# Kernel tuning notes

Hardware: AMD Instinct MI355X
Metric: run time of the kernel (lower is better)

Reference implementation:

```python
import jax, jax.numpy as jnp
import numpy as np

B, CIN, COUT, K, H, W = 16, 128, 256, 3, 56, 56
STRIDE = 1
PAD = K // 2


def setup_inputs() -> dict:
    key = jax.random.key(0)
    ks = jax.random.split(key, 12)
    x = jax.random.normal(ks[0], (B, CIN, H, W), dtype=jnp.float32)
    base_kernel = jax.random.normal(ks[1], (COUT, CIN, K, K), dtype=jnp.float32)
    bias = jnp.zeros((COUT,), dtype=jnp.float32)
    s = 1.0 / np.sqrt(CIN)
    fc_spatial_w = jax.random.uniform(ks[2], (K * K, CIN), minval=-s, maxval=s)
    fc_spatial_b = jax.random.uniform(ks[3], (K * K,), minval=-s, maxval=s)
    fc_in_w = jax.random.uniform(ks[4], (CIN, CIN), minval=-s, maxval=s)
    fc_in_b = jax.random.uniform(ks[5], (CIN,), minval=-s, maxval=s)
    fc_out_w = jax.random.uniform(ks[6], (COUT, CIN), minval=-s, maxval=s)
    fc_out_b = jax.random.uniform(ks[7], (COUT,), minval=-s, maxval=s)
    fc_kernel_w = jax.random.uniform(ks[8], (COUT * CIN * K * K, CIN), minval=-s, maxval=s)
    fc_kernel_b = jax.random.uniform(ks[9], (COUT * CIN * K * K,), minval=-s, maxval=s)
    return {
        "x": x, "base_kernel": base_kernel, "bias": bias,
        "fc_spatial_w": fc_spatial_w, "fc_spatial_b": fc_spatial_b,
        "fc_in_w": fc_in_w, "fc_in_b": fc_in_b,
        "fc_out_w": fc_out_w, "fc_out_b": fc_out_b,
        "fc_kernel_w": fc_kernel_w, "fc_kernel_b": fc_kernel_b,
    }


def _odconv(x, base_kernel, bias, fc_spatial_w, fc_spatial_b, fc_in_w, fc_in_b,
            fc_out_w, fc_out_b, fc_kernel_w, fc_kernel_b):
    b = x.shape[0]
    # global average pool -> context [B, Cin]
    context = jnp.mean(x, axis=(2, 3))
    sig = jax.nn.sigmoid
    attn_spatial = sig(context @ fc_spatial_w.T + fc_spatial_b).reshape(b, 1, 1, K, K)
    attn_in = sig(context @ fc_in_w.T + fc_in_b).reshape(b, 1, CIN, 1, 1)
    attn_out = sig(context @ fc_out_w.T + fc_out_b).reshape(b, COUT, 1, 1, 1)
    attn_kernel = sig(context @ fc_kernel_w.T + fc_kernel_b).reshape(b, COUT, CIN, K, K)
    # 5-way broadcast multiply -> per-sample dynamic kernel [B, Cout, Cin, K, K]
    dyn = base_kernel[None] * attn_out * attn_in * attn_spatial * attn_kernel

    def conv_one(xi, wi):
        # xi: [Cin, H, W], wi: [Cout, Cin, K, K]
        out = jax.lax.conv_general_dilated(
            xi[None], wi,
            window_strides=(STRIDE, STRIDE),
            padding=[(PAD, PAD), (PAD, PAD)],
            dimension_numbers=("NCHW", "OIHW", "NCHW"),
        )
        return out[0]

    out = jax.vmap(conv_one)(x, dyn)  # [B, Cout, H', W']
    return out + bias[None, :, None, None]


def reference(x, base_kernel, bias, fc_spatial_w, fc_spatial_b, fc_in_w, fc_in_b,
              fc_out_w, fc_out_b, fc_kernel_w, fc_kernel_b):
    return _odconv(x, base_kernel, bias, fc_spatial_w, fc_spatial_b, fc_in_w, fc_in_b,
                   fc_out_w, fc_out_b, fc_kernel_w, fc_kernel_b)
```

## Files before the change

### kernel.cpp

```cpp
#include <hip/hip_runtime.h>
#include <hip/hip_bf16.h>
#include <math.h>

#define BATCH 16
#define CIN   128
#define COUT  256
#define HH    56
#define WW    56
#define HW    3136
#define NTAP  9
#define NE    (COUT*CIN*NTAP)

typedef short short8 __attribute__((ext_vector_type(8)));
typedef float floatx4 __attribute__((ext_vector_type(4)));

#define WSB_CTX   0
#define WSB_ASP   8192
#define WSB_AIN   9472
#define WSB_AOUT  17664
#define WSB_XT    34048
#define WSB_DYN   (WSB_XT + BATCH*HW*CIN*2)

static __device__ inline unsigned short f2b(float f) {
    union { float f; unsigned u; } v; v.f = f;
    unsigned r = v.u + 0x7FFF + ((v.u >> 16) & 1);
    return (unsigned short)(r >> 16);
}
static __device__ inline short8 pack8(float4 a, float4 b) {
    short8 r;
    r[0] = (short)f2b(a.x); r[1] = (short)f2b(a.y); r[2] = (short)f2b(a.z); r[3] = (short)f2b(a.w);
    r[4] = (short)f2b(b.x); r[5] = (short)f2b(b.y); r[6] = (short)f2b(b.z); r[7] = (short)f2b(b.w);
    return r;
}

__global__ void k_context(const float* __restrict__ x, float* __restrict__ ctx) {
    int bc = blockIdx.x;
    const float4* p = (const float4*)(x + (size_t)bc * HW);
    float s = 0.f;
    for (int i = threadIdx.x; i < HW / 4; i += 256) { float4 v = p[i]; s += v.x + v.y + v.z + v.w; }
    for (int off = 32; off; off >>= 1) s += __shfl_down(s, off, 64);
    __shared__ float red[4];
    if ((threadIdx.x & 63) == 0) red[threadIdx.x >> 6] = s;
    __syncthreads();
    if (threadIdx.x == 0) ctx[bc] = (red[0] + red[1] + red[2] + red[3]) * (1.f / (float)HW);
}

__global__ void k_xt(const float* __restrict__ x, unsigned short* __restrict__ xt) {
    int b = blockIdx.y;
    int p = blockIdx.x * 64 + (threadIdx.x & 63);
    int icq = threadIdx.x >> 6;
    const float* xb = x + (size_t)b * CIN * HW + p;
    unsigned short tmp[32];
#pragma unroll
    for (int j = 0; j < 32; ++j) tmp[j] = f2b(xb[(size_t)(icq * 32 + j) * HW]);
    uint4* dst = (uint4*)(xt + ((size_t)b * HW + p) * CIN + icq * 32);
    const uint4* s = (const uint4*)tmp;
    dst[0] = s[0]; dst[1] = s[1]; dst[2] = s[2]; dst[3] = s[3];
}

__global__ void k_attn(const float* __restrict__ ctx,
                       const float* __restrict__ wsp, const float* __restrict__ bsp,
                       const float* __restrict__ win, const float* __restrict__ bin,
                       const float* __restrict__ wout, const float* __restrict__ bout,
                       float* __restrict__ asp, float* __restrict__ ain, float* __restrict__ aout) {
    int R = blockIdx.x * 4 + (threadIdx.x >> 6);
    int lane = threadIdx.x & 63;
    int b = R / 393, r = R % 393;
    const float* w; float bias; float* o;
    if (r < 9)        { w = wsp  + r * CIN;         bias = bsp[r];         o = asp  + b * 16  + r; }
    else if (r < 137) { w = win  + (r - 9) * CIN;   bias = bin[r - 9];     o = ain  + b * CIN + (r - 9); }
    else              { w = wout + (r - 137) * CIN; bias = bout[r - 137];  o = aout + b * COUT + (r - 137); }
    float2 wv = ((const float2*)w)[lane];
    float2 cv = ((const float2*)(ctx + b * CIN))[lane];
    float d = wv.x * cv.x + wv.y * cv.y;
    for (int off = 32; off; off >>= 1) d += __shfl_down(d, off, 64);
    if (lane == 0) *o = 1.f / (1.f + __expf(-(d + bias)));
}

__global__ void k_build(const float* __restrict__ ctx, const float* __restrict__ wk,
                        const float* __restrict__ bk, const float* __restrict__ base,
                        const float* __restrict__ asp, const float* __restrict__ ain,
                        const float* __restrict__ aout, unsigned short* __restrict__ dyn) {
    int wid = threadIdx.x >> 6, l = threadIdx.x & 63;
    int lq = l & 15, quad = l >> 4;
    short8 afr[4];
    const float* arow = ctx + lq * CIN;
#pragma unroll
    for (int kc = 0; kc < 4; ++kc) {
        float4 v0 = *(const float4*)(arow + kc * 32 + quad * 8);
        float4 v1 = *(const float4*)(arow + kc * 32 + quad * 8 + 4);
        afr[kc] = pack8(v0, v1);
    }
    int n0w = blockIdx.x * 512 + wid * 128;
    for (int nf = 0; nf < 8; ++nf) {
        int n0 = n0w + nf * 16;
        int ic  = (n0 & 127) + lq;
        int oc  = (n0 >> 7) & 255;
        int tap = n0 >> 15;
        int e = (oc * CIN + ic) * NTAP + tap;
        const float* wrow = wk + (size_t)e * CIN;
        floatx4 acc = {0.f, 0.f, 0.f, 0.f};
#pragma unroll
        for (int kc = 0; kc < 4; ++kc) {
            float4 v0 = *(const float4*)(wrow + kc * 32 + quad * 8);
            float4 v1 = *(const float4*)(wrow + kc * 32 + quad * 8 + 4);
            short8 bfr = pack8(v0, v1);
            acc = __builtin_amdgcn_mfma_f32_16x16x32_bf16(afr[kc], bfr, acc, 0, 0, 0);
        }
        float bke = bk[e], bse = base[e];
#pragma unroll
        for (int r = 0; r < 4; ++r) {
            int b = quad * 4 + r;
            float s = 1.f / (1.f + __expf(-(acc[r] + bke)));
            float v = bse * s * aout[b * COUT + oc] * ain[b * CIN + ic] * asp[b * 16 + tap];
            dyn[(size_t)b * NE + n0 + lq] = f2b(v);
        }
    }
}

__global__ __launch_bounds__(256, 2) void k_conv(
    const unsigned short* __restrict__ xt, const unsigned short* __restrict__ dyn,
    const float* __restrict__ bias, float* __restrict__ out) {
    __shared__ char s_x[348 * 80];
    __shared__ char s_a[2][128 * 80];
    int b = blockIdx.z, oc0 = blockIdx.y * 128, r0 = blockIdx.x * 4;
    int tid = threadIdx.x;
    int wid = tid >> 6, l = tid & 63, lq = l & 15, quad = l >> 4;
    int wm = wid & 1, wn = wid >> 1;
    const unsigned short* xtb  = xt  + (size_t)b * HW * CIN;
    const unsigned short* dynb = dyn + (size_t)b * NE;

    int pixaddr[7];
#pragma unroll
    for (int nf = 0; nf < 7; ++nf) {
        int n = wn * 112 + nf * 16 + lq;
        int ry = n / 56, cx = n % 56;
        pixaddr[nf] = (ry * 58 + cx) * 80 + quad * 16;
    }

    floatx4 acc[4][7];
#pragma unroll
    for (int i = 0; i < 4; ++i)
#pragma unroll
        for (int j = 0; j < 7; ++j) acc[i][j] = (floatx4){0.f, 0.f, 0.f, 0.f};

    for (int kc = 0; kc < 4; ++kc) {
        for (int u = tid; u < 1392; u += 256) {
            int icq = u & 3, pix = u >> 2;
            int ry = pix / 58, cx = pix % 58;
            int gy = r0 + ry - 1, gx = cx - 1;
            uint4 v = {0u, 0u, 0u, 0u};
            if (gy >= 0 && gy < HH && gx >= 0 && gx < WW)
                v = *(const uint4*)(xtb + (size_t)(gy * WW + gx) * CIN + kc * 32 + icq * 8);
            *(uint4*)(s_x + pix * 80 + icq * 16) = v;
        }
        for (int u = tid; u < 512; u += 256) {
            int icq = u & 3, oc = u >> 2;
            *(uint4*)(s_a[0] + oc * 80 + icq * 16) =
                *(const uint4*)(dynb + (size_t)(oc0 + oc) * CIN + kc * 32 + icq * 8);
        }
        __syncthreads();
#pragma unroll
        for (int tap = 0; tap < 9; ++tap) {
            if (tap < 8) {
                for (int u = tid; u < 512; u += 256) {
                    int icq = u & 3, oc = u >> 2;
                    *(uint4*)(s_a[(tap + 1) & 1] + oc * 80 + icq * 16) =
                        *(const uint4*)(dynb + (size_t)((tap + 1) * COUT + oc0 + oc) * CIN + kc * 32 + icq * 8);
                }
            }
            const char* sa = s_a[tap & 1];
            short8 af[4];
#pragma unroll
            for (int mf = 0; mf < 4; ++mf)
                af[mf] = *(const short8*)(sa + (wm * 64 + mf * 16 + lq) * 80 + quad * 16);
            int toff = ((tap / 3) * 58 + (tap % 3)) * 80;
#pragma unroll
            for (int nf = 0; nf < 7; ++nf) {
                short8 bf = *(const short8*)(s_x + pixaddr[nf] + toff);
#pragma unroll
                for (int mf = 0; mf < 4; ++mf)
                    acc[mf][nf] = __builtin_amdgcn_mfma_f32_16x16x32_bf16(af[mf], bf, acc[mf][nf], 0, 0, 0);
            }
            __syncthreads();
        }
    }

#pragma unroll
    for (int mf = 0; mf < 4; ++mf) {
#pragma unroll
        for (int r = 0; r < 4; ++r) {
            int oc = oc0 + wm * 64 + mf * 16 + quad * 4 + r;
            float bs = bias[oc];
            float* ob = out + (size_t)(b * COUT + oc) * HW + r0 * WW + wn * 112 + lq;
#pragma unroll
            for (int nf = 0; nf < 7; ++nf)
                ob[nf * 16] = acc[mf][nf][r] + bs;
        }
    }
}

extern "C" void kernel_launch(void* const* d_in, const int* in_sizes, int n_in,
                              void* d_out, int out_size, void* d_ws, size_t ws_size,
                              hipStream_t stream) {
    const float* x    = (const float*)d_in[0];
    const float* base = (const float*)d_in[1];
    const float* bias = (const float*)d_in[2];
    const float* wsp  = (const float*)d_in[3];
    const float* bsp  = (const float*)d_in[4];
    const float* win  = (const float*)d_in[5];
    const float* bin  = (const float*)d_in[6];
    const float* wout = (const float*)d_in[7];
    const float* bout = (const float*)d_in[8];
    const float* wk   = (const float*)d_in[9];
    const float* bk   = (const float*)d_in[10];
    float* out = (float*)d_out;
    char* ws = (char*)d_ws;

    float* ctx  = (float*)(ws + WSB_CTX);
    float* asp  = (float*)(ws + WSB_ASP);
    float* ain  = (float*)(ws + WSB_AIN);
    float* aout = (float*)(ws + WSB_AOUT);
    unsigned short* xt  = (unsigned short*)(ws + WSB_XT);
    unsigned short* dyn = (unsigned short*)(ws + WSB_DYN);

    k_context<<<BATCH * CIN, 256, 0, stream>>>(x, ctx);
    k_xt<<<dim3(HW / 64, BATCH), 256, 0, stream>>>(x, xt);
    k_attn<<<(BATCH * 393) / 4, 256, 0, stream>>>(ctx, wsp, bsp, win, bin, wout, bout, asp, ain, aout);
    k_build<<<NE / 512, 256, 0, stream>>>(ctx, wk, bk, base, asp, ain, aout, dyn);
    k_conv<<<dim3(HH / 4, COUT / 128, BATCH), 256, 0, stream>>>(xt, dyn, bias, out);
}
```

Measured before the change: 345.9 us.

## Retile conv to 8 rows x 64 channels, stage all taps per chunk

The conv kernel now covers 8 output rows by 64 output channels per block, with each wave owning two rows. Each input-channel chunk loads all 9 taps of weights into LDS at once, which removes the per-tap double-buffer loads and the per-tap barriers. The LDS row stride drops from 80 to 64 bytes, which risks more bank conflicts, and the weight-build kernel gets twice as many smaller blocks. Per-block LDS grows to about 73 KB, which may limit how many blocks fit on a CU.

Result: faster. 332.5 us (-3.9%).

```diff
diff --git a/kernel.cpp b/kernel.cpp
--- a/kernel.cpp
+++ b/kernel.cpp
@@ -91,8 +91,8 @@
         float4 v1 = *(const float4*)(arow + kc * 32 + quad * 8 + 4);
         afr[kc] = pack8(v0, v1);
     }
-    int n0w = blockIdx.x * 512 + wid * 128;
-    for (int nf = 0; nf < 8; ++nf) {
+    int n0w = blockIdx.x * 256 + wid * 64;
+    for (int nf = 0; nf < 4; ++nf) {
         int n0 = n0w + nf * 16;
         int ic  = (n0 & 127) + lq;
         int oc  = (n0 >> 7) & 255;
@@ -121,21 +121,20 @@
 __global__ __launch_bounds__(256, 2) void k_conv(
     const unsigned short* __restrict__ xt, const unsigned short* __restrict__ dyn,
     const float* __restrict__ bias, float* __restrict__ out) {
-    __shared__ char s_x[348 * 80];
-    __shared__ char s_a[2][128 * 80];
-    int b = blockIdx.z, oc0 = blockIdx.y * 128, r0 = blockIdx.x * 4;
+    __shared__ char s_x[580 * 64];
+    __shared__ char s_a[576 * 64];
+    int b = blockIdx.z, oc0 = blockIdx.y * 64, r0 = blockIdx.x * 8;
     int tid = threadIdx.x;
-    int wid = tid >> 6, l = tid & 63, lq = l & 15, quad = l >> 4;
-    int wm = wid & 1, wn = wid >> 1;
+    int wn = tid >> 6, l = tid & 63, lq = l & 15, quad = l >> 4;
     const unsigned short* xtb  = xt  + (size_t)b * HW * CIN;
     const unsigned short* dynb = dyn + (size_t)b * NE;
 
     int pixaddr[7];
 #pragma unroll
     for (int nf = 0; nf < 7; ++nf) {
-        int n = wn * 112 + nf * 16 + lq;
-        int ry = n / 56, cx = n % 56;
-        pixaddr[nf] = (ry * 58 + cx) * 80 + quad * 16;
+        int n = nf * 16 + lq;
+        int tr = wn * 2 + n / 56, col = n % 56;
+        pixaddr[nf] = (tr * 58 + col) * 64 + quad * 16;
     }
 
     floatx4 acc[4][7];
@@ -145,36 +144,29 @@
         for (int j = 0; j < 7; ++j) acc[i][j] = (floatx4){0.f, 0.f, 0.f, 0.f};
 
     for (int kc = 0; kc < 4; ++kc) {
-        for (int u = tid; u < 1392; u += 256) {
+        __syncthreads();
+        for (int u = tid; u < 2320; u += 256) {
             int icq = u & 3, pix = u >> 2;
             int ry = pix / 58, cx = pix % 58;
             int gy = r0 + ry - 1, gx = cx - 1;
             uint4 v = {0u, 0u, 0u, 0u};
             if (gy >= 0 && gy < HH && gx >= 0 && gx < WW)
                 v = *(const uint4*)(xtb + (size_t)(gy * WW + gx) * CIN + kc * 32 + icq * 8);
-            *(uint4*)(s_x + pix * 80 + icq * 16) = v;
-        }
-        for (int u = tid; u < 512; u += 256) {
-            int icq = u & 3, oc = u >> 2;
-            *(uint4*)(s_a[0] + oc * 80 + icq * 16) =
-                *(const uint4*)(dynb + (size_t)(oc0 + oc) * CIN + kc * 32 + icq * 8);
+            *(uint4*)(s_x + pix * 64 + icq * 16) = v;
+        }
+        for (int u = tid; u < 2304; u += 256) {
+            int icq = u & 3, oc = (u >> 2) & 63, tap = u >> 8;
+            *(uint4*)(s_a + u * 16) =
+                *(const uint4*)(dynb + (size_t)(tap * COUT + oc0 + oc) * CIN + kc * 32 + icq * 8);
         }
         __syncthreads();
 #pragma unroll
         for (int tap = 0; tap < 9; ++tap) {
-            if (tap < 8) {
-                for (int u = tid; u < 512; u += 256) {
-                    int icq = u & 3, oc = u >> 2;
-                    *(uint4*)(s_a[(tap + 1) & 1] + oc * 80 + icq * 16) =
-                        *(const uint4*)(dynb + (size_t)((tap + 1) * COUT + oc0 + oc) * CIN + kc * 32 + icq * 8);
-                }
-            }
-            const char* sa = s_a[tap & 1];
             short8 af[4];
 #pragma unroll
             for (int mf = 0; mf < 4; ++mf)
-                af[mf] = *(const short8*)(sa + (wm * 64 + mf * 16 + lq) * 80 + quad * 16);
-            int toff = ((tap / 3) * 58 + (tap % 3)) * 80;
+                af[mf] = *(const short8*)(s_a + (tap * 64 + mf * 16 + lq) * 64 + quad * 16);
+            int toff = ((tap / 3) * 58 + (tap % 3)) * 64;
 #pragma unroll
             for (int nf = 0; nf < 7; ++nf) {
                 short8 bf = *(const short8*)(s_x + pixaddr[nf] + toff);
@@ -182,7 +174,6 @@
                 for (int mf = 0; mf < 4; ++mf)
                     acc[mf][nf] = __builtin_amdgcn_mfma_f32_16x16x32_bf16(af[mf], bf, acc[mf][nf], 0, 0, 0);
             }
-            __syncthreads();
         }
     }
 
@@ -190,9 +181,9 @@
     for (int mf = 0; mf < 4; ++mf) {
 #pragma unroll
         for (int r = 0; r < 4; ++r) {
-            int oc = oc0 + wm * 64 + mf * 16 + quad * 4 + r;
+            int oc = oc0 + mf * 16 + quad * 4 + r;
             float bs = bias[oc];
-            float* ob = out + (size_t)(b * COUT + oc) * HW + r0 * WW + wn * 112 + lq;
+            float* ob = out + (size_t)(b * COUT + oc) * HW + (r0 + wn * 2) * 56 + lq;
 #pragma unroll
             for (int nf = 0; nf < 7; ++nf)
                 ob[nf * 16] = acc[mf][nf][r] + bs;
@@ -227,6 +218,6 @@
     k_context<<<BATCH * CIN, 256, 0, stream>>>(x, ctx);
     k_xt<<<dim3(HW / 64, BATCH), 256, 0, stream>>>(x, xt);
     k_attn<<<(BATCH * 393) / 4, 256, 0, stream>>>(ctx, wsp, bsp, win, bin, wout, bout, asp, ain, aout);
-    k_build<<<NE / 512, 256, 0, stream>>>(ctx, wk, bk, base, asp, ain, aout, dyn);
-    k_conv<<<dim3(HH / 4, COUT / 128, BATCH), 256, 0, stream>>>(xt, dyn, bias, out);
-}
+    k_build<<<NE / 256, 256, 0, stream>>>(ctx, wk, bk, base, asp, ain, aout, dyn);
+    k_conv<<<dim3(HH / 8, COUT / 64, BATCH), 256, 0, stream>>>(xt, dyn, bias, out);
+}
```
